# Performance work log

Measured on AMD Instinct MI355X. Metric: run time of the kernel, lower is better.

## Reference

```python
import math
import jax, jax.numpy as jnp
import numpy as np

NEG_INF_FILL = 1e-09  # faithful to the source: masked positions get +1e-09, not -inf

B, H, S, D = 2, 16, 2048, 64


def setup_inputs() -> dict:
    key = jax.random.key(0)
    kq, kk, kv = jax.random.split(key, 3)
    q = jax.random.normal(kq, (B, H, S, D), dtype=jnp.float32)
    k = jax.random.normal(kk, (B, H, S, D), dtype=jnp.float32)
    v = jax.random.normal(kv, (B, H, S, D), dtype=jnp.float32)
    # causal boolean mask, broadcast over heads: [B, 1, S, S]
    causal = jnp.tril(jnp.ones((S, S), dtype=bool))
    attention_mask = jnp.broadcast_to(causal[None, None, :, :], (B, 1, S, S))
    return {"q": q, "k": k, "v": v, "attention_mask": attention_mask}


def reference(q, k, v, attention_mask):
    d_k = q.shape[-1]
    # scores: [B, H, S, S]
    scores = jnp.einsum("bhqd,bhkd->bhqk", q, k) / math.sqrt(d_k)
    scores = jnp.where(attention_mask, scores, NEG_INF_FILL)
    attn = jax.nn.softmax(scores, axis=-1)
    # output: [B, H, S, D]
    return jnp.einsum("bhqk,bhkd->bhqd", attn, v)
```

## Files before the change

kernel.cpp:

```cpp
#include <hip/hip_runtime.h>


#define SEQ 2048
#define DIM 64
#define NKT 32
#define QSCALE 0.18033688011112042f

typedef _Float16 half_t;
typedef _Float16 half8  __attribute__((ext_vector_type(8)));
typedef _Float16 half4v __attribute__((ext_vector_type(4)));
typedef _Float16 half2v __attribute__((ext_vector_type(2)));
typedef float    float4v __attribute__((ext_vector_type(4)));

#define KIMG_HALFS ((size_t)4194304)
#define WS_NEED    ((size_t)17039360)

__device__ __forceinline__ void glds16(const void* g, void* l) {
    __builtin_amdgcn_global_load_lds((const __attribute__((address_space(1))) void*)g,
                                     (__attribute__((address_space(3))) void*)l,
                                     16, 0, 0);
}

__global__ __launch_bounds__(256)
void prep_kernel(const float* __restrict__ K, const float* __restrict__ V,
                 half_t* __restrict__ Kimg, half_t* __restrict__ Vimg,
                 float* __restrict__ Stab) {
    __shared__ __align__(16) half_t vt[64 * 72];
    __shared__ float part[32 * 9];
    const int bh = blockIdx.y;
    const int tid = threadIdx.x;

    if (blockIdx.x >= NKT) {
        const int dg = blockIdx.x - NKT;
        const int t = tid >> 3, dl = tid & 7;
        const int d = dg * 8 + dl;
        const float* Vb = V + (size_t)bh * SEQ * DIM;
        float s = 0.f;
        #pragma unroll 8
        for (int j = 0; j < 64; ++j) s += Vb[(size_t)(t * 64 + j) * DIM + d];
        part[t * 9 + dl] = s;
        __syncthreads();
        float r = 0.f;
        for (int tt = 31; tt >= t; --tt) r += part[tt * 9 + dl];
        Stab[((size_t)bh * 32 + t) * 64 + d] = r;
        return;
    }

    const int kt = blockIdx.x;
    const float* Kt = K + ((size_t)bh * SEQ + kt * 64) * DIM;
    const float* Vt = V + ((size_t)bh * SEQ + kt * 64) * DIM;
    half_t* Kd = Kimg + (((size_t)(bh * NKT + kt)) << 12);
    half_t* Vd = Vimg + (((size_t)(bh * NKT + kt)) << 12);

    {
        const int row = tid >> 2, q = tid & 3;
        const float* src = Kt + row * DIM + 16 * q;
        #pragma unroll
        for (int cc = 0; cc < 2; ++cc) {
            float4v a = *(const float4v*)(src + 8 * cc);
            float4v b = *(const float4v*)(src + 8 * cc + 4);
            half8 hh;
            hh[0]=(half_t)a[0]; hh[1]=(half_t)a[1]; hh[2]=(half_t)a[2]; hh[3]=(half_t)a[3];
            hh[4]=(half_t)b[0]; hh[5]=(half_t)b[1]; hh[6]=(half_t)b[2]; hh[7]=(half_t)b[3];
            const int sc = (2 * q + cc) ^ (row & 7);
            *(half8*)(Kd + row * 64 + sc * 8) = hh;
        }
    }
    {
        const int c = tid & 15, r0 = tid >> 4;
        #pragma unroll
        for (int u = 0; u < 2; ++u) {
            const float* vp = Vt + (size_t)(2 * (r0 + 16 * u)) * DIM + 4 * c;
            float4v x0 = *(const float4v*)(vp);
            float4v x1 = *(const float4v*)(vp + DIM);
            #pragma unroll
            for (int i = 0; i < 4; ++i) {
                const int d = 4 * c + i;
                vt[d * 72 + 2 * (r0 + 16 * u)]     = (half_t)x0[i];
                vt[d * 72 + 2 * (r0 + 16 * u) + 1] = (half_t)x1[i];
            }
        }
    }
    __syncthreads();
    {
        const int d = tid >> 2, g = tid & 3;
        #pragma unroll
        for (int cc = 0; cc < 2; ++cc) {
            const int c0 = 2 * g + cc;
            half8 hh = *(const half8*)(vt + d * 72 + 8 * c0);
            const int sc = c0 ^ (d & 7);
            *(half8*)(Vd + d * 64 + sc * 8) = hh;
        }
    }
}

__global__ __launch_bounds__(512, 2)
void attn_mfma_kernel(const float* __restrict__ Q,
                      const half_t* __restrict__ Kimg,
                      const half_t* __restrict__ Vimg,
                      const float* __restrict__ Stab,
                      float* __restrict__ O) {
    __shared__ __align__(16) half_t smem_h[32768];

    const int tid = threadIdx.x;
    const int l   = tid & 63;
    const int w   = tid >> 6;
    const int lx  = l & 15;
    const int h   = l >> 4;
    const int bh  = blockIdx.x;
    const int qb2 = 15 - (int)blockIdx.y;
    const int qbase = qb2 << 7;
    const int nkt = 2 * (qb2 + 1);
    const int n_tail = SEQ - (nkt << 6);

    const float* Qh = Q + (size_t)bh * SEQ * DIM;
    float*       Oh = O + (size_t)bh * SEQ * DIM;

    half8 qf[2];
    const int qrow_w = qbase + 16 * w;
    {
        const float* qp = Qh + (size_t)(qrow_w + lx) * DIM;
        #pragma unroll
        for (int s = 0; s < 2; ++s) {
            float4v a = *(const float4v*)(qp + 32 * s + 8 * h);
            float4v b = *(const float4v*)(qp + 32 * s + 8 * h + 4);
            half8 f;
            f[0] = (half_t)(a[0] * QSCALE); f[1] = (half_t)(a[1] * QSCALE);
            f[2] = (half_t)(a[2] * QSCALE); f[3] = (half_t)(a[3] * QSCALE);
            f[4] = (half_t)(b[0] * QSCALE); f[5] = (half_t)(b[1] * QSCALE);
            f[6] = (half_t)(b[2] * QSCALE); f[7] = (half_t)(b[3] * QSCALE);
            qf[s] = f;
        }
    }

    float4v acc[4];
    #pragma unroll
    for (int mt = 0; mt < 4; ++mt) acc[mt] = (float4v){0.f, 0.f, 0.f, 0.f};
    float lp = 0.f;

    const size_t tile0 = ((size_t)(bh * NKT)) << 13;
    auto stage = [&](int kt, int buf) {
        const size_t toff = tile0 + ((size_t)kt << 13);
        const char* gk = (const char*)Kimg + toff + (tid << 4);
        const char* gv = (const char*)Vimg + toff + (tid << 4);
        char* lk = (char*)smem_h + (buf << 13) + (w << 10);
        char* lv = (char*)smem_h + 24576 + (buf << 13) + (w << 10);
        glds16(gk, lk);
        glds16(gv, lv);
    };

    const int sx  = lx & 7;
    const int o0h = (h ^ sx) << 3;
    const int o1h = ((h + 4) ^ sx) << 3;
    half_t* Psw = smem_h + 24576 + (w << 10);

    stage(0, 0);
    stage(1, 1);

    int buf = 0;
    for (int kt = 0; kt < nkt; ++kt) {
        if (kt + 1 < nkt) {
            asm volatile("s_waitcnt vmcnt(2)" ::: "memory");
        } else {
            asm volatile("s_waitcnt vmcnt(0)" ::: "memory");
        }
        __syncthreads();

        if (kt + 2 < nkt) {
            int b2 = buf + 2; if (b2 >= 3) b2 -= 3;
            stage(kt + 2, b2);
        }

        const half_t* Kb = smem_h + buf * 4096 + (lx << 6);
        const half_t* Vb = smem_h + 12288 + buf * 4096 + (lx << 6);
        const int key_base = kt << 6;

        #pragma unroll
        for (int mt = 0; mt < 4; ++mt) {
            half8 ak0 = *(const half8*)(Kb + (mt << 10) + o0h);
            half8 ak1 = *(const half8*)(Kb + (mt << 10) + o1h);
            float4v ct = (float4v){0.f, 0.f, 0.f, 0.f};
            ct = __builtin_amdgcn_mfma_f32_16x16x32_f16(ak0, qf[0], ct, 0, 0, 0);
            ct = __builtin_amdgcn_mfma_f32_16x16x32_f16(ak1, qf[1], ct, 0, 0, 0);
            float pv[4];
            #pragma unroll
            for (int r = 0; r < 4; ++r)
                pv[r] = __builtin_amdgcn_exp2f(ct[r]);
            if ((key_base + 16 * mt + 15) > qrow_w) {
                const int qg = qrow_w + lx;
                const int kb = key_base + 16 * mt + 4 * h;
                #pragma unroll
                for (int r = 0; r < 4; ++r)
                    if (kb + r > qg) pv[r] = 1.0f;
            }
            lp += (pv[0] + pv[1]) + (pv[2] + pv[3]);
            half4v hp;
            hp[0] = (half_t)pv[0]; hp[1] = (half_t)pv[1];
            hp[2] = (half_t)pv[2]; hp[3] = (half_t)pv[3];
            *(half4v*)(Psw + (lx << 6)
                       + ((((mt << 1) + (h >> 1)) ^ sx) << 3) + ((h & 1) << 2)) = hp;
        }

        half8 pf0 = *(const half8*)(Psw + (lx << 6) + o0h);
        half8 pf1 = *(const half8*)(Psw + (lx << 6) + o1h);
        #pragma unroll
        for (int mtd = 0; mtd < 4; ++mtd) {
            half8 av0 = *(const half8*)(Vb + (mtd << 10) + o0h);
            half8 av1 = *(const half8*)(Vb + (mtd << 10) + o1h);
            float4v ct = acc[mtd];
            ct = __builtin_amdgcn_mfma_f32_16x16x32_f16(av0, pf0, ct, 0, 0, 0);
            ct = __builtin_amdgcn_mfma_f32_16x16x32_f16(av1, pf1, ct, 0, 0, 0);
            acc[mtd] = ct;
        }

        ++buf; if (buf >= 3) buf = 0;
    }

    float s_l = lp;
    s_l += __shfl_xor(s_l, 16, 64);
    s_l += __shfl_xor(s_l, 32, 64);
    const float linv = 1.0f / (s_l + (float)n_tail);

    float vt_l[4][4];
    if (n_tail > 0) {
        const float* Sr = Stab + (((size_t)bh << 5) + nkt) * 64;
        #pragma unroll
        for (int mt = 0; mt < 4; ++mt) {
            float4v x = *(const float4v*)(Sr + 16 * mt + 4 * h);
            vt_l[mt][0] = x[0]; vt_l[mt][1] = x[1];
            vt_l[mt][2] = x[2]; vt_l[mt][3] = x[3];
        }
    } else {
        #pragma unroll
        for (int mt = 0; mt < 4; ++mt)
            vt_l[mt][0] = vt_l[mt][1] = vt_l[mt][2] = vt_l[mt][3] = 0.f;
    }

    __syncthreads();
    float* Osm = (float*)smem_h;
    #pragma unroll
    for (int mt = 0; mt < 4; ++mt)
        #pragma unroll
        for (int r = 0; r < 4; ++r) {
            float o = (acc[mt][r] + vt_l[mt][r]) * linv;
            Osm[w * (16 * 65) + lx * 65 + 16 * mt + 4 * h + r] = o;
        }
    __syncthreads();
    {
        const int c = tid & 15, r0 = tid >> 4;
        #pragma unroll
        for (int u = 0; u < 4; ++u) {
            const int row = r0 + 32 * u;
            const int dc = 4 * c;
            const float* src = Osm + (row >> 4) * (16 * 65) + (row & 15) * 65 + dc;
            float4v ov = {src[0], src[1], src[2], src[3]};
            *(float4v*)(Oh + (size_t)(qbase + row) * DIM + dc) = ov;
        }
    }
}

#define KS_STRIDE 72
#define PS_STRIDE 72

__global__ __launch_bounds__(256, 4)
void attn_mfma_fallback(const float* __restrict__ Q,
                        const float* __restrict__ K,
                        const float* __restrict__ V,
                        float* __restrict__ O) {
    __shared__ half_t smem_h[64 * KS_STRIDE + 64 * KS_STRIDE + 4 * 16 * PS_STRIDE];
    half_t* Ks  = smem_h;
    half_t* VTs = smem_h + 64 * KS_STRIDE;
    half_t* Ps  = smem_h + 2 * 64 * KS_STRIDE;

    const int tid = threadIdx.x;
    const int l   = tid & 63;
    const int w   = tid >> 6;
    const int lx  = l & 15;
    const int h   = l >> 4;
    const int bh  = blockIdx.x;
    const int qb  = 31 - (int)blockIdx.y;
    const int qbase = qb * 64;
    const int nkt = qb + 1;
    const int n_tail = SEQ - nkt * 64;

    const float* Qh = Q + (size_t)bh * SEQ * DIM;
    const float* Kh = K + (size_t)bh * SEQ * DIM;
    const float* Vh = V + (size_t)bh * SEQ * DIM;
    float*       Oh = O + (size_t)bh * SEQ * DIM;

    half8 qf[2];
    const int qrow_w = qbase + 16 * w;
    {
        const float* qp = Qh + (size_t)(qrow_w + lx) * DIM;
        #pragma unroll
        for (int s = 0; s < 2; ++s) {
            float4v a = *(const float4v*)(qp + 32 * s + 8 * h);
            float4v b = *(const float4v*)(qp + 32 * s + 8 * h + 4);
            half8 f;
            f[0] = (half_t)(a[0] * QSCALE); f[1] = (half_t)(a[1] * QSCALE);
            f[2] = (half_t)(a[2] * QSCALE); f[3] = (half_t)(a[3] * QSCALE);
            f[4] = (half_t)(b[0] * QSCALE); f[5] = (half_t)(b[1] * QSCALE);
            f[6] = (half_t)(b[2] * QSCALE); f[7] = (half_t)(b[3] * QSCALE);
            qf[s] = f;
        }
    }

    float4v acc[4];
    #pragma unroll
    for (int mt = 0; mt < 4; ++mt) acc[mt] = (float4v){0.f, 0.f, 0.f, 0.f};
    float lp = 0.f;

    const int c  = tid & 15;
    const int r0 = tid >> 4;

    float4v kreg[4], vreg[4];
    auto load_tile = [&](int kt) {
        const float* Kt = Kh + (size_t)kt * 64 * DIM;
        const float* Vt = Vh + (size_t)kt * 64 * DIM;
        #pragma unroll
        for (int u = 0; u < 4; ++u)
            kreg[u] = *(const float4v*)(Kt + (r0 + 16 * u) * DIM + 4 * c);
        #pragma unroll
        for (int u = 0; u < 2; ++u) {
            const float* vp = Vt + (size_t)(2 * (r0 + 16 * u)) * DIM + 4 * c;
            vreg[2 * u]     = *(const float4v*)(vp);
            vreg[2 * u + 1] = *(const float4v*)(vp + DIM);
        }
    };

    load_tile(0);

    for (int kt = 0; kt < nkt; ++kt) {
        __syncthreads();
        #pragma unroll
        for (int u = 0; u < 4; ++u) {
            int kr = r0 + 16 * u;
            half4v hk;
            hk[0] = (half_t)kreg[u][0]; hk[1] = (half_t)kreg[u][1];
            hk[2] = (half_t)kreg[u][2]; hk[3] = (half_t)kreg[u][3];
            *(half4v*)(Ks + kr * KS_STRIDE + 4 * c) = hk;
        }
        #pragma unroll
        for (int u = 0; u < 2; ++u) {
            int kp = r0 + 16 * u;
            #pragma unroll
            for (int i = 0; i < 4; ++i) {
                int ir = (i + c + (c >> 2)) & 3;
                int dr = 4 * c + ir;
                half2v hv;
                hv[0] = (half_t)vreg[2 * u][ir];
                hv[1] = (half_t)vreg[2 * u + 1][ir];
                *(half2v*)(VTs + dr * KS_STRIDE + 2 * kp) = hv;
            }
        }
        __syncthreads();

        if (kt + 1 < nkt) load_tile(kt + 1);

        const int key_base = kt * 64;
        #pragma unroll
        for (int mt = 0; mt < 4; ++mt) {
            half8 ak0 = *(const half8*)(Ks + (16 * mt + lx) * KS_STRIDE + 8 * h);
            half8 ak1 = *(const half8*)(Ks + (16 * mt + lx) * KS_STRIDE + 32 + 8 * h);
            const bool need_mask = (key_base + 16 * mt + 15) > qrow_w;
            float4v ct = (float4v){0.f, 0.f, 0.f, 0.f};
            ct = __builtin_amdgcn_mfma_f32_16x16x32_f16(ak0, qf[0], ct, 0, 0, 0);
            ct = __builtin_amdgcn_mfma_f32_16x16x32_f16(ak1, qf[1], ct, 0, 0, 0);
            float p[4];
            #pragma unroll
            for (int r = 0; r < 4; ++r)
                p[r] = __builtin_amdgcn_exp2f(ct[r]);
            if (need_mask) {
                const int qg = qrow_w + lx;
                const int kb = key_base + 16 * mt + 4 * h;
                #pragma unroll
                for (int r = 0; r < 4; ++r)
                    if (kb + r > qg) p[r] = 1.0f;
            }
            lp += (p[0] + p[1]) + (p[2] + p[3]);
            half4v hp;
            hp[0] = (half_t)p[0]; hp[1] = (half_t)p[1];
            hp[2] = (half_t)p[2]; hp[3] = (half_t)p[3];
            *(half4v*)(Ps + w * (16 * PS_STRIDE) + lx * PS_STRIDE + 16 * mt + 4 * h) = hp;
        }

        half8 pf[2];
        #pragma unroll
        for (int s = 0; s < 2; ++s)
            pf[s] = *(const half8*)(Ps + w * (16 * PS_STRIDE) + lx * PS_STRIDE
                                    + 32 * s + 8 * h);
        #pragma unroll
        for (int mtd = 0; mtd < 4; ++mtd) {
            half8 av0 = *(const half8*)(VTs + (16 * mtd + lx) * KS_STRIDE + 8 * h);
            half8 av1 = *(const half8*)(VTs + (16 * mtd + lx) * KS_STRIDE + 32 + 8 * h);
            float4v ct = acc[mtd];
            ct = __builtin_amdgcn_mfma_f32_16x16x32_f16(av0, pf[0], ct, 0, 0, 0);
            ct = __builtin_amdgcn_mfma_f32_16x16x32_f16(av1, pf[1], ct, 0, 0, 0);
            acc[mtd] = ct;
        }
    }

    float s_l = lp;
    s_l += __shfl_xor(s_l, 16, 64);
    s_l += __shfl_xor(s_l, 32, 64);
    const float linv = 1.0f / (s_l + (float)n_tail);

    float ts0 = 0.f, ts1 = 0.f, ts2 = 0.f, ts3 = 0.f;
    {
        const int tstart = nkt * 64;
        #pragma unroll 4
        for (int k = tstart + r0; k < SEQ; k += 16) {
            float4v x = *(const float4v*)(Vh + (size_t)k * DIM + 4 * c);
            ts0 += x[0]; ts1 += x[1]; ts2 += x[2]; ts3 += x[3];
        }
    }
    __syncthreads();
    float* preS = (float*)smem_h;
    float* vtf  = ((float*)smem_h) + 4160;
    {
        float4v pv = {ts0, ts1, ts2, ts3};
        *(float4v*)(preS + r0 * 68 + 4 * c) = pv;
    }
    __syncthreads();
    if (tid < 64) {
        float s = 0.f;
        #pragma unroll
        for (int p = 0; p < 16; ++p) s += preS[p * 68 + tid];
        vtf[tid] = s;
    }
    __syncthreads();
    float vt_l[4][4];
    #pragma unroll
    for (int mt = 0; mt < 4; ++mt)
        #pragma unroll
        for (int r = 0; r < 4; ++r) vt_l[mt][r] = vtf[16 * mt + 4 * h + r];

    float* Osm = (float*)smem_h;
    #pragma unroll
    for (int mt = 0; mt < 4; ++mt)
        #pragma unroll
        for (int r = 0; r < 4; ++r) {
            float o = (acc[mt][r] + vt_l[mt][r]) * linv;
            Osm[w * (16 * 65) + lx * 65 + 16 * mt + 4 * h + r] = o;
        }
    __syncthreads();
    #pragma unroll
    for (int u = 0; u < 4; ++u) {
        int row = r0 + 16 * u;
        int dc = 4 * c;
        const float* src = Osm + (row >> 4) * (16 * 65) + (row & 15) * 65 + dc;
        float4v ov = {src[0], src[1], src[2], src[3]};
        *(float4v*)(Oh + (size_t)(qbase + row) * DIM + dc) = ov;
    }
}

extern "C" void kernel_launch(void* const* d_in, const int* in_sizes, int n_in,
                              void* d_out, int out_size, void* d_ws, size_t ws_size,
                              hipStream_t stream) {
    const float* q = (const float*)d_in[0];
    const float* k = (const float*)d_in[1];
    const float* v = (const float*)d_in[2];
    float* out = (float*)d_out;

    if (d_ws != nullptr && ws_size >= WS_NEED) {
        half_t* kimg = (half_t*)d_ws;
        half_t* vimg = kimg + KIMG_HALFS;
        float*  stab = (float*)((char*)d_ws + 16777216);
        prep_kernel<<<dim3(40, 32), 256, 0, stream>>>(k, v, kimg, vimg, stab);
        attn_mfma_kernel<<<dim3(32, 16), 512, 0, stream>>>(q, kimg, vimg, stab, out);
    } else {
        attn_mfma_fallback<<<dim3(32, 32), 256, 0, stream>>>(q, k, v, out);
    }
}
```

Before: 149.9 us.

## Switch attention inner loop to 32x32x16 MFMA with key-split waves

Replaces the 16x16x32 MFMA tiling with 32x32x16 MFMAs. Each pair of waves handles 32 query rows and splits the 64-key tile into two halves. The P operand is rebuilt in registers with a cross-half shuffle, so the LDS round trip for P goes away. The two key-half partial accumulators and row sums are reduced through LDS in the epilogue. LDS use drops and launch bounds are raised to 4 blocks per CU, which aims to cut LDS traffic and raise occupancy and MFMA efficiency. In exchange the epilogue gains an extra reduction and writes output with scattered scalar stores, which may be a possible memory-access concern.

```diff
diff --git a/kernel.cpp b/kernel.cpp
--- a/kernel.cpp
+++ b/kernel.cpp
@@ -10,7 +10,9 @@
 typedef _Float16 half8  __attribute__((ext_vector_type(8)));
 typedef _Float16 half4v __attribute__((ext_vector_type(4)));
 typedef _Float16 half2v __attribute__((ext_vector_type(2)));
-typedef float    float4v __attribute__((ext_vector_type(4)));
+typedef float    float4v  __attribute__((ext_vector_type(4)));
+typedef float    float16v __attribute__((ext_vector_type(16)));
+typedef int      int4v    __attribute__((ext_vector_type(4)));
 
 #define KIMG_HALFS ((size_t)4194304)
 #define WS_NEED    ((size_t)17039360)
@@ -19,6 +21,11 @@
     __builtin_amdgcn_global_load_lds((const __attribute__((address_space(1))) void*)g,
                                      (__attribute__((address_space(3))) void*)l,
                                      16, 0, 0);
+}
+
+__device__ __forceinline__ int pkh(float a, float b) {
+    half2v t; t[0] = (half_t)a; t[1] = (half_t)b;
+    return __builtin_bit_cast(int, t);
 }
 
 __global__ __launch_bounds__(256)
@@ -94,36 +101,39 @@
     }
 }
 
-__global__ __launch_bounds__(512, 2)
+__global__ __launch_bounds__(512, 4)
 void attn_mfma_kernel(const float* __restrict__ Q,
                       const half_t* __restrict__ Kimg,
                       const half_t* __restrict__ Vimg,
                       const float* __restrict__ Stab,
                       float* __restrict__ O) {
-    __shared__ __align__(16) half_t smem_h[32768];
+    __shared__ __align__(16) half_t smem_h[24576];
 
     const int tid = threadIdx.x;
     const int l   = tid & 63;
     const int w   = tid >> 6;
-    const int lx  = l & 15;
-    const int h   = l >> 4;
+    const int ln  = l & 31;
+    const int g   = l >> 5;
+    const int kh  = w & 1;
+    const int qg  = w >> 1;
     const int bh  = blockIdx.x;
     const int qb2 = 15 - (int)blockIdx.y;
     const int qbase = qb2 << 7;
     const int nkt = 2 * (qb2 + 1);
     const int n_tail = SEQ - (nkt << 6);
+    const int qrow  = qbase + 32 * qg + ln;
+    const int qwmin = qbase + 32 * qg;
 
     const float* Qh = Q + (size_t)bh * SEQ * DIM;
     float*       Oh = O + (size_t)bh * SEQ * DIM;
 
-    half8 qf[2];
-    const int qrow_w = qbase + 16 * w;
-    {
-        const float* qp = Qh + (size_t)(qrow_w + lx) * DIM;
-        #pragma unroll
-        for (int s = 0; s < 2; ++s) {
-            float4v a = *(const float4v*)(qp + 32 * s + 8 * h);
-            float4v b = *(const float4v*)(qp + 32 * s + 8 * h + 4);
+    half8 qf[4];
+    {
+        const float* qp = Qh + (size_t)qrow * DIM + 8 * g;
+        #pragma unroll
+        for (int s = 0; s < 4; ++s) {
+            float4v a = *(const float4v*)(qp + 16 * s);
+            float4v b = *(const float4v*)(qp + 16 * s + 4);
             half8 f;
             f[0] = (half_t)(a[0] * QSCALE); f[1] = (half_t)(a[1] * QSCALE);
             f[2] = (half_t)(a[2] * QSCALE); f[3] = (half_t)(a[3] * QSCALE);
@@ -133,9 +143,8 @@
         }
     }
 
-    float4v acc[4];
-    #pragma unroll
-    for (int mt = 0; mt < 4; ++mt) acc[mt] = (float4v){0.f, 0.f, 0.f, 0.f};
+    float16v acc0 = {0.f,0.f,0.f,0.f,0.f,0.f,0.f,0.f,0.f,0.f,0.f,0.f,0.f,0.f,0.f,0.f};
+    float16v acc1 = acc0;
     float lp = 0.f;
 
     const size_t tile0 = ((size_t)(bh * NKT)) << 13;
@@ -149,10 +158,8 @@
         glds16(gv, lv);
     };
 
-    const int sx  = lx & 7;
-    const int o0h = (h ^ sx) << 3;
-    const int o1h = ((h + 4) ^ sx) << 3;
-    half_t* Psw = smem_h + 24576 + (w << 10);
+    const int krow = 32 * kh + ln;
+    const int rb7  = ln & 7;
 
     stage(0, 0);
     stage(1, 1);
@@ -171,90 +178,110 @@
             stage(kt + 2, b2);
         }
 
-        const half_t* Kb = smem_h + buf * 4096 + (lx << 6);
-        const half_t* Vb = smem_h + 12288 + buf * 4096 + (lx << 6);
-        const int key_base = kt << 6;
-
-        #pragma unroll
-        for (int mt = 0; mt < 4; ++mt) {
-            half8 ak0 = *(const half8*)(Kb + (mt << 10) + o0h);
-            half8 ak1 = *(const half8*)(Kb + (mt << 10) + o1h);
-            float4v ct = (float4v){0.f, 0.f, 0.f, 0.f};
-            ct = __builtin_amdgcn_mfma_f32_16x16x32_f16(ak0, qf[0], ct, 0, 0, 0);
-            ct = __builtin_amdgcn_mfma_f32_16x16x32_f16(ak1, qf[1], ct, 0, 0, 0);
-            float pv[4];
+        const half_t* Kb = smem_h + buf * 4096;
+        const half_t* Vb = smem_h + 12288 + buf * 4096;
+
+        half8 ak0 = *(const half8*)(Kb + krow * 64 + (((0 + g) ^ rb7) << 3));
+        half8 ak1 = *(const half8*)(Kb + krow * 64 + (((2 + g) ^ rb7) << 3));
+        half8 ak2 = *(const half8*)(Kb + krow * 64 + (((4 + g) ^ rb7) << 3));
+        half8 ak3 = *(const half8*)(Kb + krow * 64 + (((6 + g) ^ rb7) << 3));
+        float16v ct = {0.f,0.f,0.f,0.f,0.f,0.f,0.f,0.f,0.f,0.f,0.f,0.f,0.f,0.f,0.f,0.f};
+        ct = __builtin_amdgcn_mfma_f32_32x32x16_f16(ak0, qf[0], ct, 0, 0, 0);
+        ct = __builtin_amdgcn_mfma_f32_32x32x16_f16(ak1, qf[1], ct, 0, 0, 0);
+        ct = __builtin_amdgcn_mfma_f32_32x32x16_f16(ak2, qf[2], ct, 0, 0, 0);
+        ct = __builtin_amdgcn_mfma_f32_32x32x16_f16(ak3, qf[3], ct, 0, 0, 0);
+
+        const int kb = (kt << 6) + 32 * kh;
+        float p[16];
+        #pragma unroll
+        for (int r = 0; r < 16; ++r)
+            p[r] = __builtin_amdgcn_exp2f(ct[r]);
+        if (kb + 31 > qwmin) {
             #pragma unroll
-            for (int r = 0; r < 4; ++r)
-                pv[r] = __builtin_amdgcn_exp2f(ct[r]);
-            if ((key_base + 16 * mt + 15) > qrow_w) {
-                const int qg = qrow_w + lx;
-                const int kb = key_base + 16 * mt + 4 * h;
-                #pragma unroll
-                for (int r = 0; r < 4; ++r)
-                    if (kb + r > qg) pv[r] = 1.0f;
+            for (int r = 0; r < 16; ++r) {
+                const int key = kb + (r & 3) + 8 * (r >> 2) + 4 * g;
+                if (key > qrow) p[r] = 1.0f;
             }
-            lp += (pv[0] + pv[1]) + (pv[2] + pv[3]);
-            half4v hp;
-            hp[0] = (half_t)pv[0]; hp[1] = (half_t)pv[1];
-            hp[2] = (half_t)pv[2]; hp[3] = (half_t)pv[3];
-            *(half4v*)(Psw + (lx << 6)
-                       + ((((mt << 1) + (h >> 1)) ^ sx) << 3) + ((h & 1) << 2)) = hp;
-        }
-
-        half8 pf0 = *(const half8*)(Psw + (lx << 6) + o0h);
-        half8 pf1 = *(const half8*)(Psw + (lx << 6) + o1h);
-        #pragma unroll
-        for (int mtd = 0; mtd < 4; ++mtd) {
-            half8 av0 = *(const half8*)(Vb + (mtd << 10) + o0h);
-            half8 av1 = *(const half8*)(Vb + (mtd << 10) + o1h);
-            float4v ct = acc[mtd];
-            ct = __builtin_amdgcn_mfma_f32_16x16x32_f16(av0, pf0, ct, 0, 0, 0);
-            ct = __builtin_amdgcn_mfma_f32_16x16x32_f16(av1, pf1, ct, 0, 0, 0);
-            acc[mtd] = ct;
+        }
+        #pragma unroll
+        for (int r = 0; r < 16; ++r) lp += p[r];
+
+        half8 af[2];
+        #pragma unroll
+        for (int sl = 0; sl < 2; ++sl) {
+            const int b = 8 * sl;
+            const int PA = pkh(p[b+0], p[b+1]);
+            const int PB = pkh(p[b+2], p[b+3]);
+            const int PC = pkh(p[b+4], p[b+5]);
+            const int PD = pkh(p[b+6], p[b+7]);
+            const int s0 = g ? PA : PC;
+            const int s1 = g ? PB : PD;
+            const int r0 = __shfl_xor(s0, 32, 64);
+            const int r1 = __shfl_xor(s1, 32, 64);
+            int4v iv;
+            iv[0] = g ? r0 : PA;
+            iv[1] = g ? r1 : PB;
+            iv[2] = g ? PC : r0;
+            iv[3] = g ? PD : r1;
+            af[sl] = __builtin_bit_cast(half8, iv);
+        }
+
+        #pragma unroll
+        for (int sl = 0; sl < 2; ++sl) {
+            const int c0 = 4 * kh + 2 * sl + g;
+            half8 bv0 = *(const half8*)(Vb + ln * 64        + ((c0 ^ rb7) << 3));
+            half8 bv1 = *(const half8*)(Vb + (32 + ln) * 64 + ((c0 ^ ((32 + ln) & 7)) << 3));
+            acc0 = __builtin_amdgcn_mfma_f32_32x32x16_f16(af[sl], bv0, acc0, 0, 0, 0);
+            acc1 = __builtin_amdgcn_mfma_f32_32x32x16_f16(af[sl], bv1, acc1, 0, 0, 0);
         }
 
         ++buf; if (buf >= 3) buf = 0;
     }
 
-    float s_l = lp;
-    s_l += __shfl_xor(s_l, 16, 64);
-    s_l += __shfl_xor(s_l, 32, 64);
-    const float linv = 1.0f / (s_l + (float)n_tail);
-
-    float vt_l[4][4];
-    if (n_tail > 0) {
-        const float* Sr = Stab + (((size_t)bh << 5) + nkt) * 64;
-        #pragma unroll
-        for (int mt = 0; mt < 4; ++mt) {
-            float4v x = *(const float4v*)(Sr + 16 * mt + 4 * h);
-            vt_l[mt][0] = x[0]; vt_l[mt][1] = x[1];
-            vt_l[mt][2] = x[2]; vt_l[mt][3] = x[3];
-        }
-    } else {
-        #pragma unroll
-        for (int mt = 0; mt < 4; ++mt)
-            vt_l[mt][0] = vt_l[mt][1] = vt_l[mt][2] = vt_l[mt][3] = 0.f;
-    }
-
-    __syncthreads();
-    float* Osm = (float*)smem_h;
-    #pragma unroll
-    for (int mt = 0; mt < 4; ++mt)
-        #pragma unroll
-        for (int r = 0; r < 4; ++r) {
-            float o = (acc[mt][r] + vt_l[mt][r]) * linv;
-            Osm[w * (16 * 65) + lx * 65 + 16 * mt + 4 * h + r] = o;
-        }
-    __syncthreads();
-    {
-        const int c = tid & 15, r0 = tid >> 4;
-        #pragma unroll
-        for (int u = 0; u < 4; ++u) {
-            const int row = r0 + 32 * u;
-            const int dc = 4 * c;
-            const float* src = Osm + (row >> 4) * (16 * 65) + (row & 15) * 65 + dc;
-            float4v ov = {src[0], src[1], src[2], src[3]};
-            *(float4v*)(Oh + (size_t)(qbase + row) * DIM + dc) = ov;
+    lp += __shfl_xor(lp, 32, 64);
+
+    __syncthreads();
+    float* abuf = (float*)smem_h;
+    float* lred = (float*)smem_h + 8192;
+    float* lbuf = (float*)smem_h + 8448;
+    if (g == 0) lred[w * 32 + ln] = lp;
+    if (kh == 1) {
+        float* ab = abuf + qg * 2048;
+        #pragma unroll
+        for (int r = 0; r < 16; ++r) {
+            ab[r * 64 + l]        = acc0[r];
+            ab[1024 + r * 64 + l] = acc1[r];
+        }
+    }
+    __syncthreads();
+
+    if (kh == 0) {
+        const float s_l = lp + lred[(w + 1) * 32 + ln];
+        const float linv = 1.0f / (s_l + (float)n_tail);
+        if (g == 0) lbuf[qg * 32 + ln] = linv;
+
+        const float* ab = abuf + qg * 2048;
+        float vt0 = 0.f, vt1 = 0.f;
+        if (n_tail > 0) {
+            const float* Sr = Stab + (((size_t)bh << 5) + nkt) * 64;
+            vt0 = Sr[ln];
+            vt1 = Sr[32 + ln];
+        }
+        float lv[16];
+        #pragma unroll
+        for (int rr = 0; rr < 4; ++rr) {
+            float4v x = *(const float4v*)(lbuf + qg * 32 + 8 * rr + 4 * g);
+            lv[4 * rr + 0] = x[0]; lv[4 * rr + 1] = x[1];
+            lv[4 * rr + 2] = x[2]; lv[4 * rr + 3] = x[3];
+        }
+        float* Ob = Oh + (size_t)(qbase + 32 * qg) * DIM;
+        #pragma unroll
+        for (int r = 0; r < 16; ++r) {
+            const int qp = (r & 3) + 8 * (r >> 2) + 4 * g;
+            const float o0 = (acc0[r] + ab[r * 64 + l] + vt0) * lv[r];
+            const float o1 = (acc1[r] + ab[1024 + r * 64 + l] + vt1) * lv[r];
+            Ob[(size_t)qp * DIM + ln]      = o0;
+            Ob[(size_t)qp * DIM + 32 + ln] = o1;
         }
     }
 }
```

Measured after the change: 146.7 us. 2.1% less time.
